# Performance work log

Measured on AMD Instinct MI355X. Metric: run time of the kernel, lower is better.

## Reference

```python
import jax, jax.numpy as jnp
import numpy as np
import math

B, Hi, Wi, D = 4, 56, 56, 256
Ho, Wo = Hi // 2, Wi // 2
HEADS, HD = D // 32, 32
NUM_ITERS, DEPTH = 3, 2
KG, KB = 3, 7
LN_EPS = 1e-5

def _ln(x, g, b):
    m = x.mean(-1, keepdims=True)
    v = ((x - m) ** 2).mean(-1, keepdims=True)
    return (x - m) * jax.lax.rsqrt(v + LN_EPS) * g + b

def _na_idx(L, K):
    # NATten neighborhood: window clamped at borders, always K neighbors
    return jnp.clip(jnp.arange(L) - K // 2, 0, L - K)[:, None] + jnp.arange(K)[None, :]

def _gather_nb(t, K):  # t [B,n,H,W,D] -> [B,n,H,K,W,K,D]
    H, W = t.shape[2], t.shape[3]
    return t[:, :, _na_idx(H, K)][:, :, :, :, _na_idx(W, K)]

def _na2d_qk(query, key, K):  # query attends to K*K neighbors of key
    b, n, H, W, d = query.shape
    return jnp.einsum('bnijd,bniajcd->bnijac', query, _gather_nb(key, K)).reshape(b, n, H, W, K * K)

def _na2d_av(attn, v, K):
    b, n, H, W, _ = attn.shape
    return jnp.einsum('bnijac,bniajcd->bnijd', attn.reshape(b, n, H, W, K, K), _gather_nb(v, K))

def _rope_cos_sin(N, hd):
    f = 1.0 / (10000.0 ** (jnp.arange(0, hd, 2, dtype=jnp.float32) / hd))
    ang = jnp.arange(N, dtype=jnp.float32)[:, None] * f[None, :]
    return jnp.cos(ang), jnp.sin(ang)

def _apply_rope(x, cos, sin):  # x [B,N,h,hd], interleaved pairs
    x2 = x.reshape(x.shape[:-1] + (-1, 2))
    x0, x1 = x2[..., 0], x2[..., 1]
    c, s = cos[None, :, None, :], sin[None, :, None, :]
    return jnp.stack([x0 * c - x1 * s, x1 * c + x0 * s], -1).reshape(x.shape)

def _forward(x, g_seed_w, g_q_w, g_k_w, g_v_w, g_mlp_w1, g_mlp_b1, g_mlp_w2, g_mlp_b2,
             g_ln_in_g, g_ln_in_b, g_ln_out_g, g_ln_out_b, g_tau, g_rpb,
             blk_ln1_g, blk_ln1_b, blk_qkv_w, blk_proj_w, blk_proj_b,
             blk_ln2_g, blk_ln2_b, blk_mlp_w1, blk_mlp_b1, blk_mlp_w2, blk_mlp_b2):
    Bx = x.shape[0]
    ln_out = lambda t: _ln(t, g_ln_out_g, g_ln_out_b)

    def to_groups(t):  # [B,N_in,D] -> [B,4,Ho,Wo,D], group p = 2*ph+pw (F.unfold 2x2 s2 order)
        m = t.reshape(Bx, Ho, 2, Wo, 2, D).transpose(0, 2, 4, 1, 3, 5)
        return m.reshape(Bx, 4, Ho, Wo, D)

    # ---- SparseGroupingLayer (local) ----
    k = to_groups(_ln(x, g_ln_in_g, g_ln_in_b) @ g_k_w.T)
    v = to_groups(x @ g_v_w.T)
    seed = jax.lax.conv_general_dilated(
        x.reshape(Bx, Hi, Wi, D), g_seed_w.transpose(2, 3, 1, 0),
        (2, 2), ((1, 1), (1, 1)), dimension_numbers=('NHWC', 'HWIO', 'NHWC'))
    x_out = ln_out(seed.reshape(Bx, Ho * Wo, D))

    ih, iw = _na_idx(Ho, KG), _na_idx(Wo, KG)
    q_idx = (ih[:, None, :, None] * Wo + iw[None, :, None, :]).reshape(-1)  # [Ho*Wo*9]
    ids_full = jnp.tile(q_idx, 4)  # same idx map for all 4 groups
    rpb = g_rpb[None, :, None, None, :]
    scale_g = jnp.exp(g_tau[0])

    for _ in range(NUM_ITERS):
        q = (ln_out(x_out) @ g_q_w.T).reshape(Bx, 1, Ho, Wo, D)
        attn = _na2d_qk(k, jnp.broadcast_to(q, (Bx, 4, Ho, Wo, D)), KG) + rpb
        attn = jax.nn.softmax(attn * scale_g, axis=-1) + 1e-6  # [B,4,Ho,Wo,9]
        col = jnp.zeros((Bx, Ho * Wo), attn.dtype).at[:, ids_full].add(attn.reshape(Bx, -1))
        denom = col[:, ids_full].reshape(Bx, 4, Ho, Wo, KG * KG)
        A_col = attn / (denom + 1e-8)
        x_out = x_out + _na2d_av(A_col, v, KG).sum(axis=1).reshape(Bx, Ho * Wo, D)
        h = jax.nn.gelu(x_out @ g_mlp_w1.T + g_mlp_b1, approximate=False) @ g_mlp_w2.T + g_mlp_b2
        x_out = x_out + ln_out(h)

    # ---- SeNaTraBlocks (local neighborhood attention, window 7, RoPE) ----
    cos, sin = _rope_cos_sin(Ho * Wo, HD)
    sc = HD ** -0.5
    for l in range(DEPTH):
        h = _ln(x_out, blk_ln1_g[l], blk_ln1_b[l])
        qkv = (h @ blk_qkv_w[l].T).reshape(Bx, Ho * Wo, 3, HEADS, HD)
        q, kk, vv = qkv[:, :, 0], qkv[:, :, 1], qkv[:, :, 2]  # [B,N,h,hd]
        q = _apply_rope(q, cos, sin).transpose(0, 2, 1, 3).reshape(Bx, HEADS, Ho, Wo, HD)
        kk = _apply_rope(kk, cos, sin).transpose(0, 2, 1, 3).reshape(Bx, HEADS, Ho, Wo, HD)
        vv = vv.transpose(0, 2, 1, 3).reshape(Bx, HEADS, Ho, Wo, HD)
        a = jax.nn.softmax(_na2d_qk(q, kk, KB) * sc, axis=-1)
        o = _na2d_av(a, vv, KB).transpose(0, 2, 3, 1, 4).reshape(Bx, Ho * Wo, D)
        x_out = x_out + (o @ blk_proj_w[l].T + blk_proj_b[l])
        h2 = _ln(x_out, blk_ln2_g[l], blk_ln2_b[l])
        m = jax.nn.gelu(h2 @ blk_mlp_w1[l].T + blk_mlp_b1[l], approximate=False) @ blk_mlp_w2[l].T + blk_mlp_b2[l]
        x_out = x_out + m
    return x_out

def setup_inputs():
    key = jax.random.key(0)
    ks = jax.random.split(key, 16)
    w = lambda k, s: jax.random.normal(k, s, dtype=jnp.float32) * 0.02
    Hm = int(D * 3.0)
    return {
        'x': jax.random.normal(ks[0], (B, Hi * Wi, D), dtype=jnp.float32),
        'g_seed_w': w(ks[1], (D, D, 3, 3)),
        'g_q_w': w(ks[2], (D, D)), 'g_k_w': w(ks[3], (D, D)), 'g_v_w': w(ks[4], (D, D)),
        'g_mlp_w1': w(ks[5], (2 * D, D)), 'g_mlp_b1': jnp.zeros((2 * D,), jnp.float32),
        'g_mlp_w2': w(ks[6], (D, 2 * D)), 'g_mlp_b2': jnp.zeros((D,), jnp.float32),
        'g_ln_in_g': jnp.ones((D,), jnp.float32), 'g_ln_in_b': jnp.zeros((D,), jnp.float32),
        'g_ln_out_g': jnp.ones((D,), jnp.float32), 'g_ln_out_b': jnp.zeros((D,), jnp.float32),
        'g_tau': jnp.full((1,), math.log(D ** -0.5), jnp.float32),
        'g_rpb': w(ks[7], (4, 9)),
        'blk_ln1_g': jnp.ones((DEPTH, D), jnp.float32), 'blk_ln1_b': jnp.zeros((DEPTH, D), jnp.float32),
        'blk_qkv_w': w(ks[8], (DEPTH, 3 * D, D)),
        'blk_proj_w': w(ks[9], (DEPTH, D, D)), 'blk_proj_b': jnp.zeros((DEPTH, D), jnp.float32),
        'blk_ln2_g': jnp.ones((DEPTH, D), jnp.float32), 'blk_ln2_b': jnp.zeros((DEPTH, D), jnp.float32),
        'blk_mlp_w1': w(ks[10], (DEPTH, Hm, D)), 'blk_mlp_b1': jnp.zeros((DEPTH, Hm), jnp.float32),
        'blk_mlp_w2': w(ks[11], (DEPTH, D, Hm)), 'blk_mlp_b2': jnp.zeros((DEPTH, D), jnp.float32),
    }

def reference(x, g_seed_w, g_q_w, g_k_w, g_v_w, g_mlp_w1, g_mlp_b1, g_mlp_w2, g_mlp_b2,
              g_ln_in_g, g_ln_in_b, g_ln_out_g, g_ln_out_b, g_tau, g_rpb,
              blk_ln1_g, blk_ln1_b, blk_qkv_w, blk_proj_w, blk_proj_b,
              blk_ln2_g, blk_ln2_b, blk_mlp_w1, blk_mlp_b1, blk_mlp_w2, blk_mlp_b2):
    return _forward(x, g_seed_w, g_q_w, g_k_w, g_v_w, g_mlp_w1, g_mlp_b1, g_mlp_w2, g_mlp_b2,
                    g_ln_in_g, g_ln_in_b, g_ln_out_g, g_ln_out_b, g_tau, g_rpb,
                    blk_ln1_g, blk_ln1_b, blk_qkv_w, blk_proj_w, blk_proj_b,
                    blk_ln2_g, blk_ln2_b, blk_mlp_w1, blk_mlp_b1, blk_mlp_w2, blk_mlp_b2)
```

## Files before the change

kernel.cpp:

```cpp
#include <hip/hip_runtime.h>
#include <hip/hip_bf16.h>
#include <math.h>

typedef __hip_bfloat16 bf16;

#define LN_EPS 1e-5f

__device__ __forceinline__ float b2f(bf16 x){ return __bfloat162float(x); }
__device__ __forceinline__ float sanit(float s){ return fminf(fmaxf(s, -80.f), 80.f); }

__device__ __forceinline__ void stc(float* p, float v){ *p = v; }
__device__ __forceinline__ void stc(bf16* p, float v){ *p = __float2bfloat16(v); }
__device__ __forceinline__ void stadd(float* p, float v){ *p += v; }
__device__ __forceinline__ void stadd(bf16* p, float v){ *p = __float2bfloat16(b2f(*p)+v); }

__device__ __forceinline__ short f2s(float f){
    union { __hip_bfloat16 h; short s; } u; u.h = __float2bfloat16(f); return u.s;
}
__device__ __forceinline__ float s2f(short s){
    union { short s; __hip_bfloat16 h; } u; u.s = s; return b2f(u.h);
}

using short8  = __attribute__((ext_vector_type(8))) short;
using floatx4 = __attribute__((ext_vector_type(4))) float;

__device__ __forceinline__ short8 load8(const float* p){
    float4 a1 = *(const float4*)p; float4 a2 = *(const float4*)(p+4);
    return (short8){ f2s(a1.x),f2s(a1.y),f2s(a1.z),f2s(a1.w),
                     f2s(a2.x),f2s(a2.y),f2s(a2.z),f2s(a2.w) };
}
__device__ __forceinline__ short8 load8(const bf16* p){ return *(const short8*)p; }

__global__ void convert_weights(const float* __restrict__ q, const float* __restrict__ k,
                                const float* __restrict__ v, const float* __restrict__ m1,
                                const float* __restrict__ m2, const float* __restrict__ qkv,
                                const float* __restrict__ proj, const float* __restrict__ bm1,
                                const float* __restrict__ bm2, bf16* __restrict__ dst)
{
    int i = blockIdx.x*256 + threadIdx.x;
    if (i >= 1769472) return;
    const float* src; int off;
    if      (i <   65536){ src=q;    off=i; }
    else if (i <  131072){ src=k;    off=i-65536; }
    else if (i <  196608){ src=v;    off=i-131072; }
    else if (i <  327680){ src=m1;   off=i-196608; }
    else if (i <  458752){ src=m2;   off=i-327680; }
    else if (i <  851968){ src=qkv;  off=i-458752; }
    else if (i <  983040){ src=proj; off=i-851968; }
    else if (i < 1376256){ src=bm1;  off=i-983040; }
    else                 { src=bm2;  off=i-1376256; }
    dst[i] = __float2bfloat16(src[off]);
}

template<typename TO>
__global__ void ln256_kernel(const float* __restrict__ in, const float* __restrict__ g,
                             const float* __restrict__ bb, TO* __restrict__ out, int addTo)
{
    int token = blockIdx.x; int d = threadIdx.x;
    int w = d >> 6, lane = d & 63;
    __shared__ float part[8];
    float v = in[(size_t)token*256 + d];
    float s = v;
    #pragma unroll
    for (int off=32; off>0; off>>=1) s += __shfl_down(s, off);
    if (lane==0) part[w] = s;
    __syncthreads();
    float mean = (part[0]+part[1]+part[2]+part[3]) * (1.f/256.f);
    float dev = v - mean;
    float q = dev*dev;
    __syncthreads();
    #pragma unroll
    for (int off=32; off>0; off>>=1) q += __shfl_down(q, off);
    if (lane==0) part[w+4] = q;
    __syncthreads();
    float var = (part[4]+part[5]+part[6]+part[7]) * (1.f/256.f);
    float r = dev*rsqrtf(var+LN_EPS)*g[d] + bb[d];
    size_t o = (size_t)token*256+d;
    if (addTo) stadd(&out[o], r); else stc(&out[o], r);
}

__global__ void ln_cast_kernel(const float* __restrict__ in, const float* __restrict__ g,
                               const float* __restrict__ bb, bf16* __restrict__ xln,
                               bf16* __restrict__ xh)
{
    int token = blockIdx.x; int d = threadIdx.x;
    int w = d >> 6, lane = d & 63;
    __shared__ float part[8];
    float v = in[(size_t)token*256 + d];
    float s = v;
    #pragma unroll
    for (int off=32; off>0; off>>=1) s += __shfl_down(s, off);
    if (lane==0) part[w] = s;
    __syncthreads();
    float mean = (part[0]+part[1]+part[2]+part[3]) * (1.f/256.f);
    float dev = v - mean;
    float q = dev*dev;
    __syncthreads();
    #pragma unroll
    for (int off=32; off>0; off>>=1) q += __shfl_down(q, off);
    if (lane==0) part[w+4] = q;
    __syncthreads();
    float var = (part[4]+part[5]+part[6]+part[7]) * (1.f/256.f);
    float r = dev*rsqrtf(var+LN_EPS)*g[d] + bb[d];
    size_t o = (size_t)token*256+d;
    xln[o] = __float2bfloat16(r);
    xh[o]  = __float2bfloat16(v);
}

__global__ void ln_add_ln(const float* __restrict__ in, const float* __restrict__ resid,
                          const float* __restrict__ g1, const float* __restrict__ b1,
                          const float* __restrict__ g2, const float* __restrict__ b2,
                          float* __restrict__ xout, bf16* __restrict__ tmph)
{
    int token = blockIdx.x; int d = threadIdx.x;
    int w = d >> 6, lane = d & 63;
    __shared__ float part[8];
    size_t o = (size_t)token*256 + d;
    float v = in[o];
    float s = v;
    #pragma unroll
    for (int off=32; off>0; off>>=1) s += __shfl_down(s, off);
    if (lane==0) part[w] = s;
    __syncthreads();
    float mean = (part[0]+part[1]+part[2]+part[3]) * (1.f/256.f);
    float dev = v - mean;
    float q = dev*dev;
    __syncthreads();
    #pragma unroll
    for (int off=32; off>0; off>>=1) q += __shfl_down(q, off);
    if (lane==0) part[w+4] = q;
    __syncthreads();
    float var = (part[4]+part[5]+part[6]+part[7]) * (1.f/256.f);
    float r = dev*rsqrtf(var+LN_EPS)*g1[d] + b1[d];
    float sx = (resid ? resid[o] : 0.f) + r;
    xout[o] = sx;
    __syncthreads();
    float s2 = sx;
    #pragma unroll
    for (int off=32; off>0; off>>=1) s2 += __shfl_down(s2, off);
    if (lane==0) part[w] = s2;
    __syncthreads();
    float mean2 = (part[0]+part[1]+part[2]+part[3]) * (1.f/256.f);
    float dev2 = sx - mean2;
    float q2 = dev2*dev2;
    __syncthreads();
    #pragma unroll
    for (int off=32; off>0; off>>=1) q2 += __shfl_down(q2, off);
    if (lane==0) part[w+4] = q2;
    __syncthreads();
    float var2 = (part[4]+part[5]+part[6]+part[7]) * (1.f/256.f);
    tmph[o] = __float2bfloat16(dev2*rsqrtf(var2+LN_EPS)*g2[d] + b2[d]);
}

template<typename TA, typename TC>
__global__ __launch_bounds__(128) void gemm_mfma(const TA* __restrict__ A,
                       const bf16* __restrict__ W,
                       const float* __restrict__ bias, const float* __restrict__ resid,
                       TC* __restrict__ C, int M, int N, int K, int do_gelu)
{
    __shared__ __align__(16) short As[2][32*40];
    __shared__ __align__(16) short Ws[2][64*40];
    int t = threadIdx.x;
    int n0 = blockIdx.x*64, m0 = blockIdx.y*32;
    int lane = t & 63, w = t >> 6;
    int quad = lane >> 4, mrow = lane & 15;
    floatx4 acc[4] = {{0,0,0,0},{0,0,0,0},{0,0,0,0},{0,0,0,0}};
    int r  = t >> 2;
    int kq = (t & 3) * 8;
    const TA*   Arow  = A + (size_t)(m0 + r)*K + kq;
    const bf16* Wrow0 = W + (size_t)(n0 + r)*K + kq;
    const bf16* Wrow1 = W + (size_t)(n0 + r + 32)*K + kq;

    short8 av  = load8(Arow);
    short8 wv0 = load8(Wrow0);
    short8 wv1 = load8(Wrow1);
    *(short8*)&As[0][r*40 + kq] = av;
    *(short8*)&Ws[0][r*40 + kq] = wv0;
    *(short8*)&Ws[0][(r+32)*40 + kq] = wv1;
    __syncthreads();

    int nb = K >> 5;
    int cur = 0;
    for (int i = 0; i < nb; i++){
        if (i+1 < nb){
            int k0 = (i+1) << 5;
            av  = load8(Arow + k0);
            wv0 = load8(Wrow0 + k0);
            wv1 = load8(Wrow1 + k0);
        }
        short8 af = *(short8*)&As[cur][(w*16 + mrow)*40 + quad*8];
        #pragma unroll
        for (int nt=0; nt<4; nt++){
            short8 bfv = *(short8*)&Ws[cur][(nt*16 + mrow)*40 + quad*8];
            acc[nt] = __builtin_amdgcn_mfma_f32_16x16x32_bf16(af, bfv, acc[nt], 0, 0, 0);
        }
        if (i+1 < nb){
            int nxt = cur ^ 1;
            *(short8*)&As[nxt][r*40 + kq] = av;
            *(short8*)&Ws[nxt][r*40 + kq] = wv0;
            *(short8*)&Ws[nxt][(r+32)*40 + kq] = wv1;
            __syncthreads();
            cur = nxt;
        }
    }
    #pragma unroll
    for (int nt=0; nt<4; nt++){
        int col = n0 + nt*16 + mrow;
        float bv = bias ? bias[col] : 0.f;
        #pragma unroll
        for (int rr=0; rr<4; rr++){
            int row = m0 + w*16 + quad*4 + rr;
            float v = acc[nt][rr] + bv;
            if (do_gelu) v = 0.5f*v*(1.0f+erff(v*0.70710678118654752f));
            size_t o = (size_t)row*N + col;
            if (resid) v += resid[o];
            stc(&C[o], v);
        }
    }
}

__global__ __launch_bounds__(128) void gemm_kv(const bf16* __restrict__ xln,
                       const bf16* __restrict__ xh, const bf16* __restrict__ wk,
                       const bf16* __restrict__ wv, bf16* __restrict__ kp,
                       bf16* __restrict__ vp)
{
    const int N = 256, K = 256;
    const bf16* A = blockIdx.z ? xh : xln;
    const bf16* W = blockIdx.z ? wv : wk;
    bf16*       C = blockIdx.z ? vp : kp;
    __shared__ __align__(16) short As[2][32*40];
    __shared__ __align__(16) short Ws[2][64*40];
    int t = threadIdx.x;
    int n0 = blockIdx.x*64, m0 = blockIdx.y*32;
    int lane = t & 63, w = t >> 6;
    int quad = lane >> 4, mrow = lane & 15;
    floatx4 acc[4] = {{0,0,0,0},{0,0,0,0},{0,0,0,0},{0,0,0,0}};
    int r  = t >> 2;
    int kq = (t & 3) * 8;
    const bf16* Arow  = A + (size_t)(m0 + r)*K + kq;
    const bf16* Wrow0 = W + (size_t)(n0 + r)*K + kq;
    const bf16* Wrow1 = W + (size_t)(n0 + r + 32)*K + kq;
    short8 av  = load8(Arow);
    short8 wv0 = load8(Wrow0);
    short8 wv1 = load8(Wrow1);
    *(short8*)&As[0][r*40 + kq] = av;
    *(short8*)&Ws[0][r*40 + kq] = wv0;
    *(short8*)&Ws[0][(r+32)*40 + kq] = wv1;
    __syncthreads();
    const int nb = K >> 5;
    int cur = 0;
    for (int i = 0; i < nb; i++){
        if (i+1 < nb){
            int k0 = (i+1) << 5;
            av  = load8(Arow + k0);
            wv0 = load8(Wrow0 + k0);
            wv1 = load8(Wrow1 + k0);
        }
        short8 af = *(short8*)&As[cur][(w*16 + mrow)*40 + quad*8];
        #pragma unroll
        for (int nt=0; nt<4; nt++){
            short8 bfv = *(short8*)&Ws[cur][(nt*16 + mrow)*40 + quad*8];
            acc[nt] = __builtin_amdgcn_mfma_f32_16x16x32_bf16(af, bfv, acc[nt], 0, 0, 0);
        }
        if (i+1 < nb){
            int nxt = cur ^ 1;
            *(short8*)&As[nxt][r*40 + kq] = av;
            *(short8*)&Ws[nxt][r*40 + kq] = wv0;
            *(short8*)&Ws[nxt][(r+32)*40 + kq] = wv1;
            __syncthreads();
            cur = nxt;
        }
    }
    #pragma unroll
    for (int nt=0; nt<4; nt++){
        int col = n0 + nt*16 + mrow;
        #pragma unroll
        for (int rr=0; rr<4; rr++){
            int row = m0 + w*16 + quad*4 + rr;
            C[(size_t)row*N + col] = __float2bfloat16(acc[nt][rr]);
        }
    }
}

__global__ void transpose_seedw(const float* __restrict__ w, bf16* __restrict__ wt)
{
    int idx = blockIdx.x*256 + threadIdx.x;
    if (idx >= 256*2304) return;
    int o = idx/2304; int rem = idx - o*2304; int pos = rem>>8; int ci = rem&255;
    wt[idx] = __float2bfloat16(w[(size_t)o*2304 + ci*9 + pos]);
}

__global__ __launch_bounds__(128) void conv_mfma(const bf16* __restrict__ xh,
                       const bf16* __restrict__ wt, float* __restrict__ C)
{
    const int K = 2304, N = 256, KC = 768;
    __shared__ __align__(16) short As[2][32*40];
    __shared__ __align__(16) short Ws[2][64*40];
    int t = threadIdx.x;
    int n0 = blockIdx.x*64, m0 = blockIdx.y*32, z = blockIdx.z;
    int lane = t & 63, w = t >> 6;
    int quad = lane >> 4, mrow = lane & 15;
    floatx4 acc[4] = {{0,0,0,0},{0,0,0,0},{0,0,0,0},{0,0,0,0}};
    int r  = t >> 2;
    int kq = (t & 3) * 8;
    int m = m0 + r;
    int wo = m%28, ho = (m/28)%28, b = m/784;
    const bf16* Wrow0 = wt + (size_t)(n0 + r)*K + z*KC + kq;
    const bf16* Wrow1 = wt + (size_t)(n0 + r + 32)*K + z*KC + kq;

    int kh = z;
    int ih = 2*ho + kh - 1;
    bool rowok = (ih>=0 && ih<56);

    auto loadA = [&](int k0)->short8{
        int kk = k0 + kq;
        int pos3 = kk >> 8;
        int ci = kk & 255;
        int iw = 2*wo + pos3 - 1;
        short8 a = {0,0,0,0,0,0,0,0};
        if (rowok && iw>=0 && iw<56)
            a = load8(xh + (((size_t)b*56 + ih)*56 + iw)*256 + ci);
        return a;
    };

    short8 av  = loadA(0);
    short8 wv0 = load8(Wrow0);
    short8 wv1 = load8(Wrow1);
    *(short8*)&As[0][r*40 + kq] = av;
    *(short8*)&Ws[0][r*40 + kq] = wv0;
    *(short8*)&Ws[0][(r+32)*40 + kq] = wv1;
    __syncthreads();

    const int nb = KC >> 5;
    int cur = 0;
    for (int i = 0; i < nb; i++){
        if (i+1 < nb){
            int k0 = (i+1) << 5;
            av  = loadA(k0);
            wv0 = load8(Wrow0 + k0);
            wv1 = load8(Wrow1 + k0);
        }
        short8 af = *(short8*)&As[cur][(w*16 + mrow)*40 + quad*8];
        #pragma unroll
        for (int nt=0; nt<4; nt++){
            short8 bfv = *(short8*)&Ws[cur][(nt*16 + mrow)*40 + quad*8];
            acc[nt] = __builtin_amdgcn_mfma_f32_16x16x32_bf16(af, bfv, acc[nt], 0, 0, 0);
        }
        if (i+1 < nb){
            int nxt = cur ^ 1;
            *(short8*)&As[nxt][r*40 + kq] = av;
            *(short8*)&Ws[nxt][r*40 + kq] = wv0;
            *(short8*)&Ws[nxt][(r+32)*40 + kq] = wv1;
            __syncthreads();
            cur = nxt;
        }
    }
    #pragma unroll
    for (int nt=0; nt<4; nt++){
        int col = n0 + nt*16 + mrow;
        #pragma unroll
        for (int rr=0; rr<4; rr++){
            int row = m0 + w*16 + quad*4 + rr;
            atomicAdd(&C[(size_t)row*N + col], acc[nt][rr]);
        }
    }
}

__global__ void grp_attn_kernel(const bf16* __restrict__ kproj, const bf16* __restrict__ qbuf,
                                const float* __restrict__ rpb, const float* __restrict__ g_tau,
                                float* __restrict__ attn, float* __restrict__ col)
{
    int idx = blockIdx.x;
    int j = idx%28; int i = (idx/28)%28; int n = (idx/784)%4; int b = idx/3136;
    int lane = threadIdx.x;
    int sh = n>>1, sw = n&1;
    const bf16* kv = kproj + ((size_t)b*3136 + (2*i+sh)*56 + (2*j+sw))*256;
    __shared__ float sc[9];
    __shared__ float sc2[9];
    int i0 = min(max(i-1,0),25), j0 = min(max(j-1,0),25);
    for (int l=0; l<9; l++){
        int qi = i0 + l/3, qj = j0 + l%3;
        const bf16* qv = qbuf + ((size_t)b*784 + qi*28+qj)*256;
        float p = 0.f;
        for (int d=lane; d<256; d+=64) p += b2f(kv[d])*b2f(qv[d]);
        for (int off=32; off>0; off>>=1) p += __shfl_down(p, off, 64);
        if (lane==0) sc[l] = p;
    }
    __syncthreads();
    if (lane==0){
        float scale = expf(g_tau[0]);
        float s[9]; float m = -1e30f;
        for (int l=0; l<9; l++){ s[l] = sanit((sc[l] + rpb[n*9+l])*scale); m = fmaxf(m, s[l]); }
        float sum = 0.f;
        for (int l=0; l<9; l++){ s[l] = expf(s[l]-m); sum += s[l]; }
        float inv = 1.f/fmaxf(sum, 1e-30f);
        for (int l=0; l<9; l++) sc2[l] = s[l]*inv + 1e-6f;
    }
    __syncthreads();
    if (lane < 9){
        float a = sc2[lane];
        attn[(size_t)idx*9 + lane] = a;
        int qi = i0 + lane/3, qj = j0 + lane%3;
        atomicAdd(&col[b*784 + qi*28 + qj], a);
    }
}

__global__ void grp_av_kernel(const float* __restrict__ attn, const float* __restrict__ col,
                              const bf16* __restrict__ vproj, float* __restrict__ xout)
{
    int idx = blockIdx.x;
    int j = idx%28; int i = (idx/28)%28; int b = idx/784;
    int d = threadIdx.x;
    int i0 = min(max(i-1,0),25), j0 = min(max(j-1,0),25);
    float acc = 0.f;
    for (int n=0; n<4; n++){
        int sh = n>>1, sw = n&1;
        const float* ap = attn + ((size_t)(b*4+n)*784 + i*28+j)*9;
        for (int l=0; l<9; l++){
            int qi = i0 + l/3, qj = j0 + l%3;
            float dv = col[b*784 + qi*28+qj] + 1e-8f;
            acc += (ap[l]/dv) * b2f(vproj[((size_t)b*3136 + (2*qi+sh)*56 + (2*qj+sw))*256 + d]);
        }
    }
    xout[(size_t)idx*256 + d] += acc;
}

__global__ __launch_bounds__(256) void blk_attn_row(const bf16* __restrict__ qkv,
                                                    bf16* __restrict__ obuf)
{
    int blk = blockIdx.x;
    int h = blk & 7; int rest = blk >> 3;
    int i = rest % 28; int b = rest / 28;
    int tid = threadIdx.x;
    int i0 = min(max(i-3,0),21);

    __shared__ float Ks[7*28*32];
    __shared__ float Vs[7*28*32];
    __shared__ float Qs[28*32];
    __shared__ float Ps[28*52];

    const float LOG1E4_16 = 0.5756462732485115f;

    for (int idx = tid; idx < 196*4; idx += 256){
        int pos = idx >> 2, u8 = idx & 3;
        int ki = i0 + pos/28, kj = pos - (pos/28)*28;
        int ttok = ki*28 + kj;
        const bf16* base = qkv + ((size_t)(b*784 + ttok))*768 + h*32 + u8*8;
        short8 k8 = *(const short8*)(base + 256);
        short8 v8 = *(const short8*)(base + 512);
        float f[8];
        #pragma unroll
        for (int d=0; d<8; d++) f[d] = s2f(k8[d]);
        #pragma unroll
        for (int m2=0; m2<4; m2++){
            int u = u8*4 + m2;
            float ang = (float)ttok * expf(-(float)u * LOG1E4_16);
            float c = cosf(ang), s = sinf(ang);
            float x0 = f[2*m2], x1 = f[2*m2+1];
            f[2*m2]   = x0*c - x1*s;
            f[2*m2+1] = x1*c + x0*s;
        }
        #pragma unroll
        for (int d=0; d<8; d++){
            Ks[pos*32 + u8*8 + d] = f[d];
            Vs[pos*32 + u8*8 + d] = s2f(v8[d]);
        }
    }
    for (int idx = tid; idx < 28*4; idx += 256){
        int tt = idx >> 2, u8 = idx & 3;
        int ttok = i*28 + tt;
        const bf16* base = qkv + ((size_t)(b*784 + ttok))*768 + h*32 + u8*8;
        short8 q8 = *(const short8*)base;
        float f[8];
        #pragma unroll
        for (int d=0; d<8; d++) f[d] = s2f(q8[d]);
        #pragma unroll
        for (int m2=0; m2<4; m2++){
            int u = u8*4 + m2;
            float ang = (float)ttok * expf(-(float)u * LOG1E4_16);
            float c = cosf(ang), s = sinf(ang);
            float x0 = f[2*m2], x1 = f[2*m2+1];
            f[2*m2]   = x0*c - x1*s;
            f[2*m2+1] = x1*c + x0*s;
        }
        #pragma unroll
        for (int d=0; d<8; d++) Qs[tt*32 + u8*8 + d] = f[d];
    }
    __syncthreads();

    int tt = tid >> 3, s = tid & 7;
    float sc[7];
    float mx = -1e30f;
    int j0 = min(max(tt-3,0),21);
    if (tt < 28){
        int c = 0;
        for (int l = s; l < 49; l += 8, c++){
            int ki = l/7, kj = j0 + l - (l/7)*7;
            const float4* kp = (const float4*)&Ks[(ki*28+kj)*32];
            const float4* qp = (const float4*)&Qs[tt*32];
            float p = 0.f;
            #pragma unroll
            for (int d=0; d<8; d++){
                float4 kv4 = kp[d], qv4 = qp[d];
                p += qv4.x*kv4.x + qv4.y*kv4.y + qv4.z*kv4.z + qv4.w*kv4.w;
            }
            sc[c] = sanit(p * 0.17677669529663687f);
            mx = fmaxf(mx, sc[c]);
        }
    }
    #pragma unroll
    for (int off=1; off<8; off<<=1) mx = fmaxf(mx, __shfl_xor(mx, off, 8));
    float sm = 0.f;
    if (tt < 28){
        int c = 0;
        for (int l = s; l < 49; l += 8, c++){ sc[c] = expf(sc[c]-mx); sm += sc[c]; }
    }
    #pragma unroll
    for (int off=1; off<8; off<<=1) sm += __shfl_xor(sm, off, 8);
    if (tt < 28){
        float inv = 1.f/fmaxf(sm, 1e-30f);
        int c = 0;
        for (int l = s; l < 49; l += 8, c++) Ps[tt*52 + l] = sc[c]*inv;
    }
    __syncthreads();

    for (int o = tid; o < 28*32; o += 256){
        int t2 = o >> 5, d = o & 31;
        int jj0 = min(max(t2-3,0),21);
        float acc = 0.f;
        #pragma unroll 7
        for (int l=0; l<49; l++){
            int ki = l/7, kj = jj0 + l - (l/7)*7;
            acc += Ps[t2*52 + l] * Vs[(ki*28+kj)*32 + d];
        }
        obuf[((size_t)(b*784 + i*28 + t2))*256 + h*32 + d] = __float2bfloat16(acc);
    }
}

extern "C" void kernel_launch(void* const* d_in, const int* in_sizes, int n_in,
                              void* d_out, int out_size, void* d_ws, size_t ws_size,
                              hipStream_t stream) {
    const float* x         = (const float*)d_in[0];
    const float* g_seed_w  = (const float*)d_in[1];
    const float* g_q_w     = (const float*)d_in[2];
    const float* g_k_w     = (const float*)d_in[3];
    const float* g_v_w     = (const float*)d_in[4];
    const float* g_mlp_w1  = (const float*)d_in[5];
    const float* g_mlp_b1  = (const float*)d_in[6];
    const float* g_mlp_w2  = (const float*)d_in[7];
    const float* g_mlp_b2  = (const float*)d_in[8];
    const float* g_ln_in_g = (const float*)d_in[9];
    const float* g_ln_in_b = (const float*)d_in[10];
    const float* g_ln_out_g= (const float*)d_in[11];
    const float* g_ln_out_b= (const float*)d_in[12];
    const float* g_tau     = (const float*)d_in[13];
    const float* g_rpb     = (const float*)d_in[14];
    const float* blk_ln1_g = (const float*)d_in[15];
    const float* blk_ln1_b = (const float*)d_in[16];
    const float* blk_qkv_w = (const float*)d_in[17];
    const float* blk_proj_w= (const float*)d_in[18];
    const float* blk_proj_b= (const float*)d_in[19];
    const float* blk_ln2_g = (const float*)d_in[20];
    const float* blk_ln2_b = (const float*)d_in[21];
    const float* blk_mlp_w1= (const float*)d_in[22];
    const float* blk_mlp_b1= (const float*)d_in[23];
    const float* blk_mlp_w2= (const float*)d_in[24];
    const float* blk_mlp_b2= (const float*)d_in[25];

    float* f      = (float*)d_ws;
    bf16*  wbuf   = (bf16*)d_ws;
    bf16*  kproj  = (bf16*)(f + 1179648);
    bf16*  vproj  = (bf16*)(f + 2785280);
    float* xout   = f + 4390912;
    float* tmp    = f + 5193728;
    bf16*  tmph   = (bf16*)(f + 5996544);
    bf16*  qbufh  = (bf16*)(f + 6397952);
    bf16*  bigh   = (bf16*)(f + 6799360);
    float* attng  = f + 8003584;
    float* col    = f + 8116480;
    bf16*  xln    = (bf16*)(f + 8119616);
    bf16*  xh     = (bf16*)(f + 9725248);

    bf16* w_q    = wbuf;
    bf16* w_k    = wbuf + 65536;
    bf16* w_v    = wbuf + 131072;
    bf16* w_m1   = wbuf + 196608;
    bf16* w_m2   = wbuf + 327680;
    bf16* w_qkv  = wbuf + 458752;
    bf16* w_proj = wbuf + 851968;
    bf16* w_bm1  = wbuf + 983040;
    bf16* w_bm2  = wbuf + 1376256;
    bf16* w_seed = wbuf + 1769472;

    convert_weights<<<6912, 256, 0, stream>>>(g_q_w, g_k_w, g_v_w, g_mlp_w1, g_mlp_w2,
                                              blk_qkv_w, blk_proj_w, blk_mlp_w1, blk_mlp_w2, wbuf);
    transpose_seedw<<<2304, 256, 0, stream>>>(g_seed_w, w_seed);
    ln_cast_kernel<<<12544, 256, 0, stream>>>(x, g_ln_in_g, g_ln_in_b, xln, xh);
    gemm_kv<<<dim3(4,392,2), 128, 0, stream>>>(xln, xh, w_k, w_v, kproj, vproj);
    hipMemsetAsync(tmp, 0, 3136*256*sizeof(float), stream);
    conv_mfma<<<dim3(4,98,3), 128, 0, stream>>>(xh, w_seed, tmp);
    ln_add_ln<<<3136, 256, 0, stream>>>(tmp, nullptr, g_ln_out_g, g_ln_out_b,
                                        g_ln_out_g, g_ln_out_b, xout, tmph);

    for (int it=0; it<3; it++){
        gemm_mfma<bf16,bf16><<<dim3(4,98), 128, 0, stream>>>(tmph, w_q, nullptr, nullptr, qbufh, 3136,256,256, 0);
        hipMemsetAsync(col, 0, 3136*sizeof(float), stream);
        grp_attn_kernel<<<12544, 64, 0, stream>>>(kproj, qbufh, g_rpb, g_tau, attng, col);
        grp_av_kernel<<<3136, 256, 0, stream>>>(attng, col, vproj, xout);
        gemm_mfma<float,bf16><<<dim3(8,98), 128, 0, stream>>>(xout, w_m1, g_mlp_b1, nullptr, bigh, 3136,512,256, 1);
        gemm_mfma<bf16,float><<<dim3(4,98), 128, 0, stream>>>(bigh, w_m2, g_mlp_b2, nullptr, tmp, 3136,256,512, 0);
        const float* g2 = (it<2) ? g_ln_out_g : blk_ln1_g;
        const float* b2 = (it<2) ? g_ln_out_b : blk_ln1_b;
        ln_add_ln<<<3136, 256, 0, stream>>>(tmp, xout, g_ln_out_g, g_ln_out_b,
                                            g2, b2, xout, tmph);
    }

    for (int l=0; l<2; l++){
        gemm_mfma<bf16,bf16><<<dim3(12,98), 128, 0, stream>>>(tmph, w_qkv + (size_t)l*196608, nullptr, nullptr, bigh, 3136,768,256, 0);
        blk_attn_row<<<896, 256, 0, stream>>>(bigh, qbufh);
        gemm_mfma<bf16,float><<<dim3(4,98), 128, 0, stream>>>(qbufh, w_proj + (size_t)l*65536, blk_proj_b + l*256, xout, xout, 3136,256,256, 0);
        ln256_kernel<bf16><<<3136, 256, 0, stream>>>(xout, blk_ln2_g + l*256, blk_ln2_b + l*256, tmph, 0);
        gemm_mfma<bf16,bf16><<<dim3(12,98), 128, 0, stream>>>(tmph, w_bm1 + (size_t)l*196608, blk_mlp_b1 + l*768, nullptr, bigh, 3136,768,256, 1);
        if (l==0){
            gemm_mfma<bf16,float><<<dim3(4,98), 128, 0, stream>>>(bigh, w_bm2, blk_mlp_b2, xout, xout, 3136,256,768, 0);
            ln256_kernel<bf16><<<3136, 256, 0, stream>>>(xout, blk_ln1_g + 256, blk_ln1_b + 256, tmph, 0);
        } else {
            gemm_mfma<bf16,float><<<dim3(4,98), 128, 0, stream>>>(bigh, w_bm2 + 196608, blk_mlp_b2 + 256, xout, (float*)d_out, 3136,256,768, 0);
        }
    }
}
```

Baseline: 573.5 us.

## Tile grouping attention per image row with shared-memory K/Q and fold memsets into kernels

Replaces the one-block-per-pixel grouping attention kernel with a per-row kernel that stages a row of keys and three rows of queries in shared memory, then computes all 28x9 scores with one thread each. This cuts redundant global reads of queries and the launch of 12544 tiny blocks. The separate memsets for the seed accumulator and the column-sum buffer are removed and their zeroing moved into the layernorm kernels, which saves launches but makes the ordering of the zeroing and the atomic accumulation depend on the stream sequence. The new kernel uses about 60 KB of shared memory, which limits occupancy.

```diff
diff --git a/kernel.cpp b/kernel.cpp
--- a/kernel.cpp
+++ b/kernel.cpp
@@ -11,8 +11,6 @@
 
 __device__ __forceinline__ void stc(float* p, float v){ *p = v; }
 __device__ __forceinline__ void stc(bf16* p, float v){ *p = __float2bfloat16(v); }
-__device__ __forceinline__ void stadd(float* p, float v){ *p += v; }
-__device__ __forceinline__ void stadd(bf16* p, float v){ *p = __float2bfloat16(b2f(*p)+v); }
 
 __device__ __forceinline__ short f2s(float f){
     union { __hip_bfloat16 h; short s; } u; u.h = __float2bfloat16(f); return u.s;
@@ -76,12 +74,12 @@
     float var = (part[4]+part[5]+part[6]+part[7]) * (1.f/256.f);
     float r = dev*rsqrtf(var+LN_EPS)*g[d] + bb[d];
     size_t o = (size_t)token*256+d;
-    if (addTo) stadd(&out[o], r); else stc(&out[o], r);
+    if (addTo) out[o] += r; else stc(&out[o], r);
 }
 
 __global__ void ln_cast_kernel(const float* __restrict__ in, const float* __restrict__ g,
                                const float* __restrict__ bb, bf16* __restrict__ xln,
-                               bf16* __restrict__ xh)
+                               bf16* __restrict__ xh, float* __restrict__ tmpz)
 {
     int token = blockIdx.x; int d = threadIdx.x;
     int w = d >> 6, lane = d & 63;
@@ -105,17 +103,20 @@
     size_t o = (size_t)token*256+d;
     xln[o] = __float2bfloat16(r);
     xh[o]  = __float2bfloat16(v);
+    if (token < 3136) tmpz[(size_t)token*256 + d] = 0.f;
 }
 
 __global__ void ln_add_ln(const float* __restrict__ in, const float* __restrict__ resid,
                           const float* __restrict__ g1, const float* __restrict__ b1,
                           const float* __restrict__ g2, const float* __restrict__ b2,
-                          float* __restrict__ xout, bf16* __restrict__ tmph)
+                          float* __restrict__ xout, bf16* __restrict__ tmph,
+                          float* __restrict__ colz)
 {
     int token = blockIdx.x; int d = threadIdx.x;
     int w = d >> 6, lane = d & 63;
     __shared__ float part[8];
     size_t o = (size_t)token*256 + d;
+    if (d == 0) colz[token] = 0.f;
     float v = in[o];
     float s = v;
     #pragma unroll
@@ -366,41 +367,67 @@
     }
 }
 
-__global__ void grp_attn_kernel(const bf16* __restrict__ kproj, const bf16* __restrict__ qbuf,
+__global__ __launch_bounds__(256) void grp_attn_row(const bf16* __restrict__ kproj,
+                                const bf16* __restrict__ qbuf,
                                 const float* __restrict__ rpb, const float* __restrict__ g_tau,
                                 float* __restrict__ attn, float* __restrict__ col)
 {
-    int idx = blockIdx.x;
-    int j = idx%28; int i = (idx/28)%28; int n = (idx/784)%4; int b = idx/3136;
-    int lane = threadIdx.x;
+    int blk = blockIdx.x;
+    int i = blk % 28; int bn = blk / 28; int n = bn & 3; int b = bn >> 2;
+    int tid = threadIdx.x;
     int sh = n>>1, sw = n&1;
-    const bf16* kv = kproj + ((size_t)b*3136 + (2*i+sh)*56 + (2*j+sw))*256;
-    __shared__ float sc[9];
-    __shared__ float sc2[9];
-    int i0 = min(max(i-1,0),25), j0 = min(max(j-1,0),25);
-    for (int l=0; l<9; l++){
+    int i0 = min(max(i-1,0),25);
+    __shared__ short Ks[28*256];
+    __shared__ short Qs[3*28*256];
+    __shared__ float sc[28*9];
+    __shared__ float pr[28*9];
+
+    for (int u = tid; u < 28*32; u += 256){
+        int j = u >> 5, c = u & 31;
+        *(short8*)&Ks[j*256 + c*8] =
+            *(const short8*)(kproj + ((size_t)b*3136 + (2*i+sh)*56 + (2*j+sw))*256 + c*8);
+    }
+    for (int u = tid; u < 3*28*32; u += 256){
+        int r = u / (28*32); int rem = u - r*(28*32);
+        int j = rem >> 5, c = rem & 31;
+        *(short8*)&Qs[(r*28 + j)*256 + c*8] =
+            *(const short8*)(qbuf + ((size_t)b*784 + (i0+r)*28 + j)*256 + c*8);
+    }
+    __syncthreads();
+
+    float scale = expf(g_tau[0]);
+    if (tid < 252){
+        int pix = tid / 9, l = tid - (tid/9)*9;
+        int j0 = min(max(pix-1,0),25);
+        int qr = l/3, qj = j0 + (l - qr*3);
+        const short* kp = &Ks[pix*256];
+        const short* qp = &Qs[(qr*28 + qj)*256];
+        float p = 0.f;
+        for (int c = 0; c < 32; c++){
+            short8 k8 = *(const short8*)(kp + c*8);
+            short8 q8 = *(const short8*)(qp + c*8);
+            #pragma unroll
+            for (int d=0; d<8; d++) p += s2f(k8[d])*s2f(q8[d]);
+        }
+        sc[pix*9 + l] = sanit((p + rpb[n*9+l])*scale);
+    }
+    __syncthreads();
+    if (tid < 28){
+        float m = -1e30f;
+        for (int l=0;l<9;l++) m = fmaxf(m, sc[tid*9+l]);
+        float sum=0.f; float e[9];
+        for (int l=0;l<9;l++){ e[l]=expf(sc[tid*9+l]-m); sum+=e[l]; }
+        float inv = 1.f/fmaxf(sum,1e-30f);
+        for (int l=0;l<9;l++) pr[tid*9+l] = e[l]*inv + 1e-6f;
+    }
+    __syncthreads();
+    if (tid < 252){
+        int pix = tid/9, l = tid - (tid/9)*9;
+        float a = pr[pix*9+l];
+        int idx = (b*4+n)*784 + i*28 + pix;
+        attn[(size_t)idx*9 + l] = a;
+        int j0 = min(max(pix-1,0),25);
         int qi = i0 + l/3, qj = j0 + l%3;
-        const bf16* qv = qbuf + ((size_t)b*784 + qi*28+qj)*256;
-        float p = 0.f;
-        for (int d=lane; d<256; d+=64) p += b2f(kv[d])*b2f(qv[d]);
-        for (int off=32; off>0; off>>=1) p += __shfl_down(p, off, 64);
-        if (lane==0) sc[l] = p;
-    }
-    __syncthreads();
-    if (lane==0){
-        float scale = expf(g_tau[0]);
-        float s[9]; float m = -1e30f;
-        for (int l=0; l<9; l++){ s[l] = sanit((sc[l] + rpb[n*9+l])*scale); m = fmaxf(m, s[l]); }
-        float sum = 0.f;
-        for (int l=0; l<9; l++){ s[l] = expf(s[l]-m); sum += s[l]; }
-        float inv = 1.f/fmaxf(sum, 1e-30f);
-        for (int l=0; l<9; l++) sc2[l] = s[l]*inv + 1e-6f;
-    }
-    __syncthreads();
-    if (lane < 9){
-        float a = sc2[lane];
-        attn[(size_t)idx*9 + lane] = a;
-        int qi = i0 + lane/3, qj = j0 + lane%3;
         atomicAdd(&col[b*784 + qi*28 + qj], a);
     }
 }
@@ -595,24 +622,22 @@
     convert_weights<<<6912, 256, 0, stream>>>(g_q_w, g_k_w, g_v_w, g_mlp_w1, g_mlp_w2,
                                               blk_qkv_w, blk_proj_w, blk_mlp_w1, blk_mlp_w2, wbuf);
     transpose_seedw<<<2304, 256, 0, stream>>>(g_seed_w, w_seed);
-    ln_cast_kernel<<<12544, 256, 0, stream>>>(x, g_ln_in_g, g_ln_in_b, xln, xh);
+    ln_cast_kernel<<<12544, 256, 0, stream>>>(x, g_ln_in_g, g_ln_in_b, xln, xh, tmp);
     gemm_kv<<<dim3(4,392,2), 128, 0, stream>>>(xln, xh, w_k, w_v, kproj, vproj);
-    hipMemsetAsync(tmp, 0, 3136*256*sizeof(float), stream);
     conv_mfma<<<dim3(4,98,3), 128, 0, stream>>>(xh, w_seed, tmp);
     ln_add_ln<<<3136, 256, 0, stream>>>(tmp, nullptr, g_ln_out_g, g_ln_out_b,
-                                        g_ln_out_g, g_ln_out_b, xout, tmph);
+                                        g_ln_out_g, g_ln_out_b, xout, tmph, col);
 
     for (int it=0; it<3; it++){
         gemm_mfma<bf16,bf16><<<dim3(4,98), 128, 0, stream>>>(tmph, w_q, nullptr, nullptr, qbufh, 3136,256,256, 0);
-        hipMemsetAsync(col, 0, 3136*sizeof(float), stream);
-        grp_attn_kernel<<<12544, 64, 0, stream>>>(kproj, qbufh, g_rpb, g_tau, attng, col);
+        grp_attn_row<<<448, 256, 0, stream>>>(kproj, qbufh, g_rpb, g_tau, attng, col);
         grp_av_kernel<<<3136, 256, 0, stream>>>(attng, col, vproj, xout);
         gemm_mfma<float,bf16><<<dim3(8,98), 128, 0, stream>>>(xout, w_m1, g_mlp_b1, nullptr, bigh, 3136,512,256, 1);
         gemm_mfma<bf16,float><<<dim3(4,98), 128, 0, stream>>>(bigh, w_m2, g_mlp_b2, nullptr, tmp, 3136,256,512, 0);
         const float* g2 = (it<2) ? g_ln_out_g : blk_ln1_g;
         const float* b2 = (it<2) ? g_ln_out_b : blk_ln1_b;
         ln_add_ln<<<3136, 256, 0, stream>>>(tmp, xout, g_ln_out_g, g_ln_out_b,
-                                            g2, b2, xout, tmph);
+                                            g2, b2, xout, tmph, col);
     }
 
     for (int l=0; l<2; l++){
```

Result: faster. 517.2 us (-9.8%).
